# Performance work log

Measured on AMD Instinct MI355X. Metric: run time of the kernel, lower is better.

The kernel has to match this reference:

```python
import jax, jax.numpy as jnp
import numpy as np


def setup_inputs() -> dict:
    key = jax.random.key(0)
    k1, k2 = jax.random.split(key)
    # x: [B, emb_dim, H, W] encoder features; embed: [emb_dim, dict_size] codebook
    x = jax.random.normal(k1, (32, 256, 32, 32), dtype=jnp.float32)
    embed = jax.random.normal(k2, (256, 8192), dtype=jnp.float32)
    return {"x": x, "embed": embed}


def reference(x, embed):
    B, C, H, W = x.shape  # C == emb_dim
    # torch transpose(1, -1) swaps dims 1 and 3 -> [B, W, H, C]
    flatten = jnp.transpose(x, (0, 3, 2, 1)).reshape(-1, C)  # [N, C], N = B*W*H
    # L2 distance via expansion: ||e||^2 + ||z||^2 - 2 z e  -> [N, dict_size]
    dist = (jnp.sum(embed * embed, axis=0)[None, :]
            + jnp.sum(flatten * flatten, axis=1, keepdims=True)
            - 2.0 * flatten @ embed)
    # nearest codebook id per vector; original views ids back as input shape minus dim 1
    ids = jnp.argmin(dist, axis=1).reshape(B, H, W)  # int ids, [B, H, W]
    # embedding lookup from embed.T ([dict_size, C]) -> [B, H, W, C]
    vqs = embed.T[ids]
    # torch transpose(1, -1) on 4D -> [B, C, W, H] (matches x since H == W)
    vqs = jnp.transpose(vqs, (0, 3, 2, 1))
    # straight-through estimator: forward value = vqs, grad w.r.t. x = identity
    out = vqs + x - jax.lax.stop_gradient(x)
    return out, ids
```

## Files before the change

kernel.cpp:

```cpp
#include <hip/hip_runtime.h>
#include <math.h>

typedef float f32x4 __attribute__((ext_vector_type(4)));
typedef __attribute__((ext_vector_type(8))) short short8;

#define C_DIM  256
#define K_DIM  8192
#define HW     1024
#define N_ROWS 32768
#define N_OUT  8388608
#define TAU    0.75f

__device__ __forceinline__ unsigned short f2bf(float v) {
    union { float f; unsigned u; } a; a.f = v;
    unsigned r = a.u + 0x7fffu + ((a.u >> 16) & 1u);
    return (unsigned short)(r >> 16);
}
__device__ __forceinline__ float bf2f(unsigned short b) {
    union { float f; unsigned u; } a; a.u = ((unsigned)b) << 16; return a.f;
}


__global__ void prepA_kernel(const float* __restrict__ x, unsigned short* __restrict__ abuf) {
    __shared__ float ldsT[256 * 65];
    const int tid = threadIdx.x;
    const int b = blockIdx.x >> 4, tq = blockIdx.x & 15;
    const int t0 = tq << 6;
    const int l = tid & 63, q = tid >> 6;
    const float* xb = x + ((size_t)b << 18) + t0;
    #pragma unroll 8
    for (int cg = 0; cg < 64; ++cg) {
        int c = (cg << 2) + q;
        ldsT[c * 65 + l] = xb[((size_t)c << 10) + l];
    }
    __syncthreads();
    const int slabblk = (b << 2) + (tq >> 2);
    const int fbase = (tq & 3) << 2;
    #pragma unroll
    for (int i = 0; i < 8; ++i) {
        int unit = (i << 2) + q;
        int ck = unit >> 2, fsub = unit & 3;
        int toff = (fsub << 4) + (l & 15);
        int ch0 = (ck << 5) + ((l >> 4) << 3);
        short8 hi;
        #pragma unroll
        for (int j = 0; j < 8; ++j) hi[j] = (short)f2bf(ldsT[(ch0 + j) * 65 + toff]);
        size_t base = (((size_t)slabblk * 8 + ck) * 16 + fbase + fsub) * 512 + l * 8;
        *(short8*)(abuf + base) = hi;
    }
}

__global__ void prepE_kernel(const float* __restrict__ embed, unsigned short* __restrict__ ebuf,
                             float* __restrict__ e_norm, float* __restrict__ embedT) {
    __shared__ float ldsT[256 * 65];
    __shared__ float pnorm[256];
    const int tid = threadIdx.x;
    const int kq = blockIdx.x;
    const int col0 = kq << 6;
    const int l = tid & 63, q = tid >> 6;
    #pragma unroll 8
    for (int cg = 0; cg < 64; ++cg) {
        int c = (cg << 2) + q;
        ldsT[c * 65 + l] = embed[((size_t)c << 13) + col0 + l];
    }
    __syncthreads();
    {
        float s = 0.f;
        #pragma unroll 8
        for (int cc = 0; cc < 64; ++cc) {
            float v = ldsT[(q * 64 + cc) * 65 + l];
            s = __builtin_fmaf(v, v, s);
        }
        pnorm[q * 64 + l] = s;
    }
    __syncthreads();
    if (tid < 64)
        e_norm[col0 + tid] = (pnorm[tid] + pnorm[64 + tid]) + (pnorm[128 + tid] + pnorm[192 + tid]);
    #pragma unroll
    for (int i = 0; i < 16; ++i) {
        int unit = (i << 2) + q;
        int f = unit & 3, s = (unit >> 2) & 1, ck = unit >> 3;
        int coff = (f << 4) + (l & 15);
        int ch0 = (ck << 5) + ((l >> 4) << 3);
        short8 w;
        #pragma unroll
        for (int j = 0; j < 8; ++j) {
            float v = ldsT[(ch0 + j) * 65 + coff];
            unsigned short h = f2bf(v);
            w[j] = (short)(s ? f2bf(v - bf2f(h)) : h);
        }
        size_t base = ((((size_t)kq * 8 + ck) * 2 + s) * 4 + f) * 512 + l * 8;
        *(short8*)(ebuf + base) = w;
    }
    if (embedT) {
        #pragma unroll 8
        for (int i = 0; i < 64; ++i)
            embedT[(size_t)(col0 + i) * 256 + tid] = ldsT[tid * 65 + i];
    }
}

#define GLDS(S, D) __builtin_amdgcn_global_load_lds(                              \
        (const __attribute__((address_space(1))) void*)(S),                       \
        (__attribute__((address_space(3))) void*)(D), 16, 0, 0)

__launch_bounds__(512, 2)
__global__ void vq_main(const unsigned short* __restrict__ abuf,
                        const unsigned short* __restrict__ ebuf,
                        const float* __restrict__ e_norm,
                        float4* __restrict__ res) {
    __shared__ unsigned short ldsA[49152];
    __shared__ unsigned short ldsE[3][8192];
    const int tid  = threadIdx.x;
    const int lane = tid & 63;
    const int wid  = tid >> 6;
    const int wm   = wid >> 1, wn = wid & 1;
    const int mtB  = blockIdx.x >> 1, nh = blockIdx.x & 1;
    const unsigned short* aSlab = abuf + (size_t)mtB * 65536u;

    #define STAGE_E(NTL, KK, BUF) do {                                                        \
        GLDS(ebuf + ((size_t)(nh * 64 + (NTL)) * 32768u) + (KK) * 4096 + tid * 8,             \
             &ldsE[BUF][tid * 8]);                                                            \
        GLDS(ebuf + ((size_t)(nh * 64 + 32 + (NTL)) * 32768u) + (KK) * 4096 + tid * 8,        \
             &ldsE[BUF][4096 + tid * 8]);                                                     \
    } while (0)

    #pragma unroll
    for (int i = 0; i < 12; ++i)
        GLDS(aSlab + i * 4096 + tid * 8, ldsA + i * 4096 + tid * 8);
    STAGE_E(0, 0, 0);

    short8 a6[4], a7[4];
    #pragma unroll
    for (int mi = 0; mi < 4; ++mi) {
        a6[mi] = *(const short8*)(aSlab + 6 * 8192 + (wm * 4 + mi) * 512 + lane * 8);
        a7[mi] = *(const short8*)(aSlab + 7 * 8192 + (wm * 4 + mi) * 512 + lane * 8);
    }

    float d1[16], d2[16]; int i1[16], i2[16];
    #pragma unroll
    for (int s = 0; s < 16; ++s) { d1[s] = INFINITY; d2[s] = INFINITY; i1[s] = 0; i2[s] = 0; }

    asm volatile("s_waitcnt vmcnt(0)" ::: "memory");
    __syncthreads();
    STAGE_E(0, 1, 1);

    int cur = 0;
    #pragma unroll 1
    for (int ntl = 0; ntl < 32; ++ntl) {
        const int colb = nh * 4096 + wn * 2048 + ntl * 64 + (lane & 15);
        float e2v[4];
        f32x4 acc[4][4];
        #pragma unroll
        for (int mi = 0; mi < 4; ++mi)
            #pragma unroll
            for (int cf = 0; cf < 4; ++cf) acc[mi][cf] = (f32x4){0.f, 0.f, 0.f, 0.f};

        #pragma unroll
        for (int kk = 0; kk < 8; ++kk) {
            if (kk == 7 && ntl == 31) { asm volatile("s_waitcnt vmcnt(0)" ::: "memory"); }
            else                      { asm volatile("s_waitcnt vmcnt(2)" ::: "memory"); }
            __builtin_amdgcn_s_barrier();
            asm volatile("" ::: "memory");

            if (kk == 0) {
                #pragma unroll
                for (int cf = 0; cf < 4; ++cf) e2v[cf] = e_norm[colb + cf * 16];
            }
            const int np = ntl * 8 + kk + 2;
            if (np < 256) {
                int nb = cur + 2; if (nb >= 3) nb -= 3;
                STAGE_E(np >> 3, np & 7, nb);
            }

            short8 ah[4];
            if (kk < 6) {
                #pragma unroll
                for (int mi = 0; mi < 4; ++mi)
                    ah[mi] = *(const short8*)(ldsA + kk * 8192 + (wm * 4 + mi) * 512 + lane * 8);
            } else if (kk == 6) {
                #pragma unroll
                for (int mi = 0; mi < 4; ++mi) ah[mi] = a6[mi];
            } else {
                #pragma unroll
                for (int mi = 0; mi < 4; ++mi) ah[mi] = a7[mi];
            }
            const unsigned short* le = ldsE[cur];
            short8 eh[4], el[4];
            #pragma unroll
            for (int cf = 0; cf < 4; ++cf) {
                eh[cf] = *(const short8*)(le + wn * 4096 + cf * 512 + lane * 8);
                el[cf] = *(const short8*)(le + wn * 4096 + 2048 + cf * 512 + lane * 8);
            }
            __builtin_amdgcn_s_setprio(1);
            #pragma unroll
            for (int cf = 0; cf < 4; ++cf)
                #pragma unroll
                for (int mi = 0; mi < 4; ++mi) {
                    acc[mi][cf] = __builtin_amdgcn_mfma_f32_16x16x32_bf16(ah[mi], eh[cf], acc[mi][cf], 0, 0, 0);
                    acc[mi][cf] = __builtin_amdgcn_mfma_f32_16x16x32_bf16(ah[mi], el[cf], acc[mi][cf], 0, 0, 0);
                }
            __builtin_amdgcn_s_setprio(0);
            cur = (cur == 2) ? 0 : cur + 1;
        }

        #pragma unroll
        for (int cf = 0; cf < 4; ++cf) {
            const int idx = colb + cf * 16;
            #pragma unroll
            for (int mi = 0; mi < 4; ++mi)
                #pragma unroll
                for (int r = 0; r < 4; ++r) {
                    const int s = mi * 4 + r;
                    float d = __builtin_fmaf(-2.f, acc[mi][cf][r], e2v[cf]);
                    bool b1 = d < d1[s];
                    bool b2 = d < d2[s];
                    d2[s] = b1 ? d1[s] : (b2 ? d : d2[s]);
                    i2[s] = b1 ? i1[s] : (b2 ? idx : i2[s]);
                    d1[s] = b1 ? d : d1[s];
                    i1[s] = b1 ? idx : i1[s];
                }
        }
    }

    #pragma unroll
    for (int s = 0; s < 16; ++s) {
        float a1 = d1[s], a2 = d2[s]; int x1 = i1[s], x2 = i2[s];
        #pragma unroll
        for (int m = 1; m < 8; m <<= 1) {
            float o1 = __shfl_xor(a1, m, 64), o2 = __shfl_xor(a2, m, 64);
            int  oi1 = __shfl_xor(x1, m, 64), oi2 = __shfl_xor(x2, m, 64);
            bool ow = (o1 < a1) || (o1 == a1 && oi1 < x1);
            float w1v = ow ? o1 : a1; int w1i = ow ? oi1 : x1;
            float l1  = ow ? a1 : o1; int l1i = ow ? x1 : oi1;
            float c2  = ow ? o2 : a2; int c2i = ow ? oi2 : x2;
            bool sw = (c2 < l1) || (c2 == l1 && c2i < l1i);
            a1 = w1v; x1 = w1i;
            a2 = sw ? c2 : l1; x2 = sw ? c2i : l1i;
        }
        d1[s] = a1; d2[s] = a2; i1[s] = x1; i2[s] = x2;
    }
    if ((lane & 7) == 0) {
        const int lst = (lane >> 3) & 1;
        const int h = lane >> 4;
        const int slot = nh * 4 + wn * 2 + lst;
        const int rowbase = (mtB << 8) + wm * 64 + (h << 2);
        #pragma unroll
        for (int mi = 0; mi < 4; ++mi)
            #pragma unroll
            for (int r = 0; r < 4; ++r) {
                const int s = mi * 4 + r;
                int row = rowbase + mi * 16 + r;
                float4 v; v.x = d1[s]; v.y = d2[s];
                v.z = __int_as_float(i1[s]); v.w = __int_as_float(i2[s]);
                res[row * 8 + slot] = v;
            }
    }
    #undef STAGE_E
}

__global__ void merge_kernel(const float* __restrict__ x, const float* __restrict__ embed,
                             const float* __restrict__ e_norm,
                             const float4* __restrict__ res, int* __restrict__ ids_final) {
    int row = blockIdx.x * 256 + threadIdx.x;
    float4 v[8];
    #pragma unroll
    for (int j = 0; j < 8; ++j) v[j] = res[row * 8 + j];
    float w1 = INFINITY; int wi = 0x7fffffff;
    #pragma unroll
    for (int j = 0; j < 8; ++j) {
        float d = v[j].x; int i = __float_as_int(v[j].z);
        if (d < w1 || (d == w1 && i < wi)) { w1 = d; wi = i; }
    }
    float w2 = INFINITY;
    #pragma unroll
    for (int j = 0; j < 8; ++j) {
        if (__float_as_int(v[j].z) != wi && v[j].x < w2) w2 = v[j].x;
        if (__float_as_int(v[j].w) != wi && v[j].y < w2) w2 = v[j].y;
    }
    int id = wi;
    if (w2 - w1 <= TAU) {
        int b = row >> 10, t = row & 1023;
        const float* xb = x + ((size_t)b << 18) + t;
        float bd = INFINITY; int bi = 0x7fffffff;
        float thr = w1 + TAU;
        #pragma unroll
        for (int j = 0; j < 8; ++j)
            #pragma unroll
            for (int sl = 0; sl < 2; ++sl) {
                float dap = sl ? v[j].y : v[j].x;
                int k = __float_as_int(sl ? v[j].w : v[j].z);
                if (dap <= thr) {
                    float dot = 0.f;
                    for (int c = 0; c < C_DIM; ++c)
                        dot = __builtin_fmaf(xb[(size_t)c << 10], embed[((size_t)c << 13) + k], dot);
                    float dd = __fadd_rn(e_norm[k], -__fmul_rn(2.0f, dot));
                    if (dd < bd || (dd == bd && k < bi)) { bd = dd; bi = k; }
                }
            }
        id = bi;
    }
    ids_final[row] = id;
}

__global__ void outT_kernel(const float* __restrict__ embedT, const int* __restrict__ ids_final,
                            float* __restrict__ out, float* __restrict__ ids_out) {
    __shared__ float fo[64 * 257];
    __shared__ int idsl[64];
    const int blk = blockIdx.x;
    const int b = blk >> 4, t0 = (blk & 15) << 6;
    const int tid = threadIdx.x;
    const int l = tid & 63, q = tid >> 6;
    if (tid < 64) {
        int t = t0 + tid;
        int id = ids_final[(b << 10) + t];
        idsl[tid] = id;
        int n = (b << 10) + ((t & 31) << 5) + (t >> 5);
        ids_out[n] = (float)id;
    }
    __syncthreads();
    #pragma unroll
    for (int i = 0; i < 16; ++i) {
        int slot = (i << 2) + q;
        const float* src = embedT + (size_t)idsl[slot] * 256;
        #pragma unroll
        for (int seg = 0; seg < 4; ++seg)
            fo[slot * 257 + (seg << 6) + l] = src[(seg << 6) + l];
    }
    __syncthreads();
    float* ob = out + ((size_t)b << 18) + t0;
    #pragma unroll 8
    for (int ci = 0; ci < 64; ++ci) {
        int c = (ci << 2) + q;
        ob[((size_t)c << 10) + l] = fo[l * 257 + c];
    }
}

__global__ void out_kernel(const float* __restrict__ embed, const int* __restrict__ ids_final,
                           float* __restrict__ out, float* __restrict__ ids_out) {
    const int blk = blockIdx.x;
    const int b = blk >> 4, t0 = (blk & 15) << 6;
    const int tid = threadIdx.x;
    const int t_off = tid & 63, w4 = tid >> 6;
    if (tid < 64) {
        int t = t0 + tid;
        int id = ids_final[(b << 10) + t];
        int n = (b << 10) + ((t & 31) << 5) + (t >> 5);
        ids_out[n] = (float)id;
    }
    const int myid = ids_final[(b << 10) + t0 + t_off];
    const float* ecol = embed + myid;
    float* ob = out + b * (C_DIM * HW) + t0 + t_off;
    #pragma unroll 4
    for (int c = w4; c < C_DIM; c += 4)
        ob[c * HW] = ecol[c * K_DIM];
}

extern "C" void kernel_launch(void* const* d_in, const int* in_sizes, int n_in,
                              void* d_out, int out_size, void* d_ws, size_t ws_size,
                              hipStream_t stream) {
    const float* x     = (const float*)d_in[0];
    const float* embed = (const float*)d_in[1];
    float* out = (float*)d_out;
    float* ids_out = out + N_OUT;

    unsigned short* abuf = (unsigned short*)d_out;
    float4* res = (float4*)((char*)d_out + (16u << 20));

    unsigned short* ebuf = (unsigned short*)d_ws;
    float* e_norm    = (float*)((char*)d_ws + 8388608u);
    int*   ids_final = (int*)((char*)d_ws + 8388608u + 32768u);
    size_t embT_off  = 8388608u + 32768u + 131072u;
    bool useT = (ws_size >= embT_off + 8388608u);
    float* embedT = useT ? (float*)((char*)d_ws + embT_off) : nullptr;

    prepA_kernel<<<512, 256, 0, stream>>>(x, abuf);
    prepE_kernel<<<128, 256, 0, stream>>>(embed, ebuf, e_norm, embedT);
    vq_main<<<256, 512, 0, stream>>>(abuf, ebuf, e_norm, res);
    merge_kernel<<<N_ROWS / 256, 256, 0, stream>>>(x, embed, e_norm, res, ids_final);
    if (useT) outT_kernel<<<512, 256, 0, stream>>>(embedT, ids_final, out, ids_out);
    else      out_kernel<<<512, 256, 0, stream>>>(embed, ids_final, out, ids_out);
}
```

Baseline: 533.1 us.

## Load codebook fragments directly into registers and remap blocks for XCD locality

The codebook tile is no longer staged through a triple-buffered LDS ring with per-step barriers. Each wave now loads its own E fragments straight from global memory into registers, double-buffered across k-steps, and the whole A slab lives in LDS. Block indices are also remapped so blocks on the same XCD share the same codebook half, which should improve L2 reuse. This removes the barriers and the LDS round-trip for E, but raises register pressure and relies on cache hits to hide global load latency with no explicit wait control.

```diff
diff --git a/kernel.cpp b/kernel.cpp
--- a/kernel.cpp
+++ b/kernel.cpp
@@ -108,47 +108,47 @@
                         const unsigned short* __restrict__ ebuf,
                         const float* __restrict__ e_norm,
                         float4* __restrict__ res) {
-    __shared__ unsigned short ldsA[49152];
-    __shared__ unsigned short ldsE[3][8192];
+    __shared__ unsigned short ldsA[65536];
     const int tid  = threadIdx.x;
     const int lane = tid & 63;
     const int wid  = tid >> 6;
     const int wm   = wid >> 1, wn = wid & 1;
-    const int mtB  = blockIdx.x >> 1, nh = blockIdx.x & 1;
+    const int bid  = blockIdx.x;
+    const int xcd  = bid & 7;
+    const int nh   = xcd >> 2;
+    const int mtB  = ((bid >> 3) << 2) + (xcd & 3);
     const unsigned short* aSlab = abuf + (size_t)mtB * 65536u;
 
-    #define STAGE_E(NTL, KK, BUF) do {                                                        \
-        GLDS(ebuf + ((size_t)(nh * 64 + (NTL)) * 32768u) + (KK) * 4096 + tid * 8,             \
-             &ldsE[BUF][tid * 8]);                                                            \
-        GLDS(ebuf + ((size_t)(nh * 64 + 32 + (NTL)) * 32768u) + (KK) * 4096 + tid * 8,        \
-             &ldsE[BUF][4096 + tid * 8]);                                                     \
-    } while (0)
-
-    #pragma unroll
-    for (int i = 0; i < 12; ++i)
+    #pragma unroll
+    for (int i = 0; i < 16; ++i)
         GLDS(aSlab + i * 4096 + tid * 8, ldsA + i * 4096 + tid * 8);
-    STAGE_E(0, 0, 0);
-
-    short8 a6[4], a7[4];
-    #pragma unroll
-    for (int mi = 0; mi < 4; ++mi) {
-        a6[mi] = *(const short8*)(aSlab + 6 * 8192 + (wm * 4 + mi) * 512 + lane * 8);
-        a7[mi] = *(const short8*)(aSlab + 7 * 8192 + (wm * 4 + mi) * 512 + lane * 8);
-    }
+
+    const size_t ntBase = (size_t)(nh * 64 + wn * 32);
 
     float d1[16], d2[16]; int i1[16], i2[16];
     #pragma unroll
     for (int s = 0; s < 16; ++s) { d1[s] = INFINITY; d2[s] = INFINITY; i1[s] = 0; i2[s] = 0; }
 
+    short8 eha[4], ela[4], ehb[4], elb[4];
+    {
+        const unsigned short* src = ebuf + ntBase * 32768u + lane * 8;
+        #pragma unroll
+        for (int cf = 0; cf < 4; ++cf) {
+            eha[cf] = *(const short8*)(src + cf * 512);
+            ela[cf] = *(const short8*)(src + 2048 + cf * 512);
+        }
+    }
+
     asm volatile("s_waitcnt vmcnt(0)" ::: "memory");
     __syncthreads();
-    STAGE_E(0, 1, 1);
-
-    int cur = 0;
+
     #pragma unroll 1
     for (int ntl = 0; ntl < 32; ++ntl) {
         const int colb = nh * 4096 + wn * 2048 + ntl * 64 + (lane & 15);
         float e2v[4];
+        #pragma unroll
+        for (int cf = 0; cf < 4; ++cf) e2v[cf] = e_norm[colb + cf * 16];
+
         f32x4 acc[4][4];
         #pragma unroll
         for (int mi = 0; mi < 4; ++mi)
@@ -156,51 +156,55 @@
             for (int cf = 0; cf < 4; ++cf) acc[mi][cf] = (f32x4){0.f, 0.f, 0.f, 0.f};
 
         #pragma unroll
-        for (int kk = 0; kk < 8; ++kk) {
-            if (kk == 7 && ntl == 31) { asm volatile("s_waitcnt vmcnt(0)" ::: "memory"); }
-            else                      { asm volatile("s_waitcnt vmcnt(2)" ::: "memory"); }
-            __builtin_amdgcn_s_barrier();
-            asm volatile("" ::: "memory");
-
-            if (kk == 0) {
-                #pragma unroll
-                for (int cf = 0; cf < 4; ++cf) e2v[cf] = e_norm[colb + cf * 16];
+        for (int kks = 0; kks < 4; ++kks) {
+            {
+                const int np = ntl * 8 + 2 * kks + 1;
+                const unsigned short* nsrc =
+                    ebuf + (ntBase + (np >> 3)) * 32768u + (np & 7) * 4096 + lane * 8;
+                #pragma unroll
+                for (int cf = 0; cf < 4; ++cf) {
+                    ehb[cf] = *(const short8*)(nsrc + cf * 512);
+                    elb[cf] = *(const short8*)(nsrc + 2048 + cf * 512);
+                }
+                short8 ah[4];
+                #pragma unroll
+                for (int mi = 0; mi < 4; ++mi)
+                    ah[mi] = *(const short8*)(ldsA + (2 * kks) * 8192 + (wm * 4 + mi) * 512 + lane * 8);
+                __builtin_amdgcn_s_setprio(1);
+                #pragma unroll
+                for (int cf = 0; cf < 4; ++cf)
+                    #pragma unroll
+                    for (int mi = 0; mi < 4; ++mi) {
+                        acc[mi][cf] = __builtin_amdgcn_mfma_f32_16x16x32_bf16(ah[mi], eha[cf], acc[mi][cf], 0, 0, 0);
+                        acc[mi][cf] = __builtin_amdgcn_mfma_f32_16x16x32_bf16(ah[mi], ela[cf], acc[mi][cf], 0, 0, 0);
+                    }
+                __builtin_amdgcn_s_setprio(0);
             }
-            const int np = ntl * 8 + kk + 2;
-            if (np < 256) {
-                int nb = cur + 2; if (nb >= 3) nb -= 3;
-                STAGE_E(np >> 3, np & 7, nb);
+            {
+                const int np = ntl * 8 + 2 * kks + 2;
+                if (np < 256) {
+                    const unsigned short* nsrc =
+                        ebuf + (ntBase + (np >> 3)) * 32768u + (np & 7) * 4096 + lane * 8;
+                    #pragma unroll
+                    for (int cf = 0; cf < 4; ++cf) {
+                        eha[cf] = *(const short8*)(nsrc + cf * 512);
+                        ela[cf] = *(const short8*)(nsrc + 2048 + cf * 512);
+                    }
+                }
+                short8 ah[4];
+                #pragma unroll
+                for (int mi = 0; mi < 4; ++mi)
+                    ah[mi] = *(const short8*)(ldsA + (2 * kks + 1) * 8192 + (wm * 4 + mi) * 512 + lane * 8);
+                __builtin_amdgcn_s_setprio(1);
+                #pragma unroll
+                for (int cf = 0; cf < 4; ++cf)
+                    #pragma unroll
+                    for (int mi = 0; mi < 4; ++mi) {
+                        acc[mi][cf] = __builtin_amdgcn_mfma_f32_16x16x32_bf16(ah[mi], ehb[cf], acc[mi][cf], 0, 0, 0);
+                        acc[mi][cf] = __builtin_amdgcn_mfma_f32_16x16x32_bf16(ah[mi], elb[cf], acc[mi][cf], 0, 0, 0);
+                    }
+                __builtin_amdgcn_s_setprio(0);
             }
-
-            short8 ah[4];
-            if (kk < 6) {
-                #pragma unroll
-                for (int mi = 0; mi < 4; ++mi)
-                    ah[mi] = *(const short8*)(ldsA + kk * 8192 + (wm * 4 + mi) * 512 + lane * 8);
-            } else if (kk == 6) {
-                #pragma unroll
-                for (int mi = 0; mi < 4; ++mi) ah[mi] = a6[mi];
-            } else {
-                #pragma unroll
-                for (int mi = 0; mi < 4; ++mi) ah[mi] = a7[mi];
-            }
-            const unsigned short* le = ldsE[cur];
-            short8 eh[4], el[4];
-            #pragma unroll
-            for (int cf = 0; cf < 4; ++cf) {
-                eh[cf] = *(const short8*)(le + wn * 4096 + cf * 512 + lane * 8);
-                el[cf] = *(const short8*)(le + wn * 4096 + 2048 + cf * 512 + lane * 8);
-            }
-            __builtin_amdgcn_s_setprio(1);
-            #pragma unroll
-            for (int cf = 0; cf < 4; ++cf)
-                #pragma unroll
-                for (int mi = 0; mi < 4; ++mi) {
-                    acc[mi][cf] = __builtin_amdgcn_mfma_f32_16x16x32_bf16(ah[mi], eh[cf], acc[mi][cf], 0, 0, 0);
-                    acc[mi][cf] = __builtin_amdgcn_mfma_f32_16x16x32_bf16(ah[mi], el[cf], acc[mi][cf], 0, 0, 0);
-                }
-            __builtin_amdgcn_s_setprio(0);
-            cur = (cur == 2) ? 0 : cur + 1;
         }
 
         #pragma unroll
@@ -255,7 +259,6 @@
                 res[row * 8 + slot] = v;
             }
     }
-    #undef STAGE_E
 }
 
 __global__ void merge_kernel(const float* __restrict__ x, const float* __restrict__ embed,
```

Measured after the change: 678.5 us. +27.3%, slower.
